# Kernel optimization log

Hardware: AMD Instinct MI355X
Metric: run time of the kernel (lower is better)

The kernel has to match this reference:

```python
import jax, jax.numpy as jnp
import numpy as np
import math

D_MODEL = 1024
NUM_HEADS = 16
HEAD_DIM = D_MODEL // NUM_HEADS


def setup_inputs() -> dict:
    key = jax.random.key(0)
    ks = jax.random.split(key, 9)
    B, S = 2, 2048
    scale = 1.0 / math.sqrt(D_MODEL)
    x = jax.random.normal(ks[0], (B, S, D_MODEL), dtype=jnp.float32)
    # torch nn.Linear params: weight [out, in], bias [out]
    Wq = jax.random.normal(ks[1], (D_MODEL, D_MODEL), dtype=jnp.float32) * scale
    bq = jax.random.normal(ks[2], (D_MODEL,), dtype=jnp.float32) * scale
    Wk = jax.random.normal(ks[3], (D_MODEL, D_MODEL), dtype=jnp.float32) * scale
    bk = jax.random.normal(ks[4], (D_MODEL,), dtype=jnp.float32) * scale
    Wv = jax.random.normal(ks[5], (D_MODEL, D_MODEL), dtype=jnp.float32) * scale
    bv = jax.random.normal(ks[6], (D_MODEL,), dtype=jnp.float32) * scale
    Wo = jax.random.normal(ks[7], (D_MODEL, D_MODEL), dtype=jnp.float32) * scale
    bo = jax.random.normal(ks[8], (D_MODEL,), dtype=jnp.float32) * scale
    return {"x": x, "Wq": Wq, "bq": bq, "Wk": Wk, "bk": bk,
            "Wv": Wv, "bv": bv, "Wo": Wo, "bo": bo}


def reference(x, Wq, bq, Wk, bk, Wv, bv, Wo, bo):
    B, S, _ = x.shape
    H, Dh = NUM_HEADS, HEAD_DIM

    def proj(W, b):
        # torch Linear: x @ W.T + b -> [B,S,D] -> [B,H,S,Dh]
        y = jnp.einsum('bsd,ed->bse', x, W) + b
        return y.reshape(B, S, H, Dh).transpose(0, 2, 1, 3)

    Q = proj(Wq, bq)
    K = proj(Wk, bk)
    V = proj(Wv, bv)

    # scores [B,H,S,S], causal mask with -inf, then scale by 1/sqrt(head_dim)
    scores = jnp.einsum('bhqd,bhkd->bhqk', Q, K)
    causal = jnp.tril(jnp.ones((S, S), dtype=bool))
    scores = jnp.where(causal, scores, -jnp.inf)
    A = jax.nn.softmax(scores / math.sqrt(Dh), axis=-1)

    O = jnp.einsum('bhqk,bhkd->bhqd', A, V)  # [B,H,S,Dh]
    O = O.transpose(0, 2, 1, 3).reshape(B, S, H * Dh)
    return jnp.einsum('bsd,ed->bse', O, Wo) + bo
```

## Files before the change

### kernel.cpp

```cpp
#include <hip/hip_runtime.h>


typedef _Float16 f16x8 __attribute__((ext_vector_type(8)));
typedef _Float16 f16x4 __attribute__((ext_vector_type(4)));
typedef _Float16 f16x2 __attribute__((ext_vector_type(2)));
typedef float f32x4 __attribute__((ext_vector_type(4)));

#define S_  2048
#define DM  1024
#define NH  16
#define DH  64

__device__ __forceinline__ void gload_lds16(const void* g, void* s) {
  __builtin_amdgcn_global_load_lds(
      (const __attribute__((address_space(1))) void*)g,
      (__attribute__((address_space(3))) void*)s, 16, 0, 0);
}

__device__ __forceinline__ f16x2 pkrtz(float a, float b) {
  return __builtin_bit_cast(f16x2, __builtin_amdgcn_cvt_pkrtz(a, b));
}


__global__ void cvt_x_kernel(const float* __restrict__ src,
                             _Float16* __restrict__ dst) {
  const int i = blockIdx.x * 256 + threadIdx.x;
  const float4 v = ((const float4*)src)[i];
  f16x4 h;
  h[0] = (_Float16)v.x; h[1] = (_Float16)v.y;
  h[2] = (_Float16)v.z; h[3] = (_Float16)v.w;
  ((f16x4*)dst)[i] = h;
}

__global__ void cvt_w_kernel(const float* __restrict__ w0,
                             const float* __restrict__ w1,
                             const float* __restrict__ w2,
                             const float* __restrict__ w3,
                             _Float16* __restrict__ dst) {
  const int y = blockIdx.y;
  const float* src = (y == 0) ? w0 : (y == 1) ? w1 : (y == 2) ? w2 : w3;
  const int i = blockIdx.x * 256 + threadIdx.x;
  const float4 v = ((const float4*)src)[i];
  f16x4 h;
  h[0] = (_Float16)v.x; h[1] = (_Float16)v.y;
  h[2] = (_Float16)v.z; h[3] = (_Float16)v.w;
  ((f16x4*)(dst + (size_t)y * (DM * DM)))[i] = h;
}


__device__ __forceinline__ void gemm_core_k1024(
    const _Float16* __restrict__ A, const _Float16* __restrict__ W,
    _Float16* As, _Float16* Ws, f32x4 acc[4][4], int m0, int n0)
{
  const int t = threadIdx.x;
  const int w = t >> 6, l = t & 63;
  const int quad = l >> 4, ln = l & 15;
  const int wm = (w >> 1) << 6, wn = (w & 1) << 6;
  const int srow = l >> 2, scol = (l & 3) << 3;

  for (int k0 = 0; k0 < DM; k0 += 32) {
#pragma unroll
    for (int i = 0; i < 2; ++i) {
      const int ra = w * 32 + i * 16;
      gload_lds16(&A[(size_t)(m0 + ra + srow) * DM + k0 + scol], &As[ra * 32]);
      gload_lds16(&W[(size_t)(n0 + ra + srow) * DM + k0 + scol], &Ws[ra * 32]);
    }
    __syncthreads();

    f16x8 af[4], bf[4];
#pragma unroll
    for (int mi = 0; mi < 4; ++mi)
      af[mi] = *(const f16x8*)&As[(wm + mi * 16 + ln) * 32 + quad * 8];
#pragma unroll
    for (int ni = 0; ni < 4; ++ni)
      bf[ni] = *(const f16x8*)&Ws[(wn + ni * 16 + ln) * 32 + quad * 8];
#pragma unroll
    for (int mi = 0; mi < 4; ++mi)
#pragma unroll
      for (int ni = 0; ni < 4; ++ni)
        acc[mi][ni] = __builtin_amdgcn_mfma_f32_16x16x32_f16(
            af[mi], bf[ni], acc[mi][ni], 0, 0, 0);
    __syncthreads();
  }
}

__global__ __launch_bounds__(256, 2) void gemm_qkv_kernel(
    const _Float16* __restrict__ xb, const _Float16* __restrict__ wb,
    const float* __restrict__ bq, const float* __restrict__ bk,
    const float* __restrict__ bv, _Float16* __restrict__ qkv)
{
  __shared__ _Float16 As[128 * 32];
  __shared__ _Float16 Ws[128 * 32];
  const int z = blockIdx.z;
  const _Float16* W = wb + (size_t)z * (DM * DM);
  const float* bias = (z == 0) ? bq : ((z == 1) ? bk : bv);
  _Float16* out = qkv + (size_t)z * 4194304;

  const f32x4 z4 = {0.f, 0.f, 0.f, 0.f};
  f32x4 acc[4][4];
#pragma unroll
  for (int mi = 0; mi < 4; ++mi)
#pragma unroll
    for (int ni = 0; ni < 4; ++ni) acc[mi][ni] = z4;

  const int m0 = blockIdx.y * 128, n0 = blockIdx.x * 128;
  gemm_core_k1024(xb, W, As, Ws, acc, m0, n0);

  const int t = threadIdx.x, w = t >> 6, l = t & 63;
  const int quad = l >> 4, ln = l & 15;
  const int wm = (w >> 1) << 6, wn = (w & 1) << 6;
  const float scale = (z == 0) ? 0.18033688f : 1.0f;

#pragma unroll
  for (int ni = 0; ni < 4; ++ni) {
    const int c = n0 + wn + ni * 16 + ln;
    const float bias_c = bias[c];
    const int h = c >> 6, d = c & 63;
#pragma unroll
    for (int mi = 0; mi < 4; ++mi) {
      const int mb = m0 + wm + mi * 16 + quad * 4;
#pragma unroll
      for (int r = 0; r < 4; ++r) {
        const int mg = mb + r;
        const int b = mg >> 11, s = mg & 2047;
        const int bh = b * NH + h;
        const float v = (acc[mi][ni][r] + bias_c) * scale;
        size_t idx;
        if (z == 2)
          idx = (size_t)bh * 131072 + (s >> 5) * 2048 + (d >> 4) * 512 +
                ((s >> 3) & 3) * 128 + (d & 15) * 8 + (s & 7);
        else
          idx = (size_t)bh * 131072 + (s >> 4) * 1024 + (d >> 5) * 512 +
                ((d >> 3) & 3) * 128 + (s & 15) * 8 + (d & 7);
        out[idx] = (_Float16)v;
      }
    }
  }
}

__global__ __launch_bounds__(256, 2) void gemm_out_kernel(
    const _Float16* __restrict__ ob, const _Float16* __restrict__ wo,
    const float* __restrict__ bo, float* __restrict__ out)
{
  __shared__ _Float16 As[128 * 32];
  __shared__ _Float16 Ws[128 * 32];
  const f32x4 z4 = {0.f, 0.f, 0.f, 0.f};
  f32x4 acc[4][4];
#pragma unroll
  for (int mi = 0; mi < 4; ++mi)
#pragma unroll
    for (int ni = 0; ni < 4; ++ni) acc[mi][ni] = z4;

  const int m0 = blockIdx.y * 128, n0 = blockIdx.x * 128;
  gemm_core_k1024(ob, wo, As, Ws, acc, m0, n0);

  const int t = threadIdx.x, w = t >> 6, l = t & 63;
  const int quad = l >> 4, ln = l & 15;
  const int wm = (w >> 1) << 6, wn = (w & 1) << 6;

#pragma unroll
  for (int ni = 0; ni < 4; ++ni) {
    const int c = n0 + wn + ni * 16 + ln;
    const float bias_c = bo[c];
#pragma unroll
    for (int mi = 0; mi < 4; ++mi) {
      const int mb = m0 + wm + mi * 16 + quad * 4;
#pragma unroll
      for (int r = 0; r < 4; ++r)
        out[(size_t)(mb + r) * DM + c] = acc[mi][ni][r] + bias_c;
    }
  }
}


struct KVfrag { f16x8 k[4]; f16x8 v[4]; };

__device__ __forceinline__ KVfrag load_tile(const _Float16* __restrict__ kb_,
                                            const _Float16* __restrict__ vb_,
                                            int t, int l) {
  KVfrag f;
#pragma unroll
  for (int i = 0; i < 4; ++i)
    f.k[i] = *(const f16x8*)(kb_ + (size_t)(t * 4 + i) * 512 + l * 8);
#pragma unroll
  for (int i = 0; i < 4; ++i)
    f.v[i] = *(const f16x8*)(vb_ + (size_t)(t * 4 + i) * 512 + l * 8);
  return f;
}

template <bool DIAG>
__device__ __forceinline__ void compute_tile(
    const KVfrag& kv, const f16x8 (&qf)[2][2], f32x4 (&oacc)[4][2],
    float (&l_i)[2], _Float16* Ps, int quad, int ln)
{
  const f32x4 z4 = {0.f, 0.f, 0.f, 0.f};
  f32x4 sacc[2][2];
#pragma unroll
  for (int mi = 0; mi < 2; ++mi)
#pragma unroll
    for (int qc = 0; qc < 2; ++qc) sacc[mi][qc] = z4;

#pragma unroll
  for (int ks = 0; ks < 2; ++ks)
#pragma unroll
    for (int mi = 0; mi < 2; ++mi)
#pragma unroll
      for (int qc = 0; qc < 2; ++qc)
        sacc[mi][qc] = __builtin_amdgcn_mfma_f32_16x16x32_f16(
            kv.k[mi * 2 + ks], qf[qc][ks], sacc[mi][qc], 0, 0, 0);

  const int sw = (ln & 3) << 1;
#pragma unroll
  for (int qc = 0; qc < 2; ++qc) {
    float rs = 0.f;
#pragma unroll
    for (int mi = 0; mi < 2; ++mi) {
      float p[4];
#pragma unroll
      for (int r = 0; r < 4; ++r) {
        p[r] = __builtin_amdgcn_exp2f(sacc[mi][qc][r]);
        if (DIAG && (mi * 16 + quad * 4 + r > qc * 16 + ln)) p[r] = 0.f;
        rs += p[r];
      }
      const f16x2 lo = pkrtz(p[0], p[1]);
      const f16x2 hi = pkrtz(p[2], p[3]);
      const f16x4 pk = __builtin_shufflevector(lo, hi, 0, 1, 2, 3);
      const int g = (mi * 4 + quad) ^ sw;
      *(f16x4*)&Ps[(qc * 16 + ln) * 40 + g * 4] = pk;
    }
    rs += __shfl_xor(rs, 16);
    rs += __shfl_xor(rs, 32);
    l_i[qc] += rs;
  }

  f16x8 pb[2];
#pragma unroll
  for (int qc = 0; qc < 2; ++qc) {
    const int g2 = (quad * 2) ^ sw;
    pb[qc] = *(const f16x8*)&Ps[(qc * 16 + ln) * 40 + g2 * 4];
  }

#pragma unroll
  for (int di = 0; di < 4; ++di)
#pragma unroll
    for (int qc = 0; qc < 2; ++qc)
      oacc[di][qc] = __builtin_amdgcn_mfma_f32_16x16x32_f16(
          kv.v[di], pb[qc], oacc[di][qc], 0, 0, 0);
}

__global__ __launch_bounds__(128, 2) void attn_kernel(
    const _Float16* __restrict__ QF, const _Float16* __restrict__ KF,
    const _Float16* __restrict__ VF, _Float16* __restrict__ Ob)
{
  __shared__ _Float16 Ps[2 * 32 * 40];
  __shared__ float mrg[64 * 34];

  const int i = blockIdx.x;
  const int bh = ((i & 7) << 2) | ((i >> 3) & 3);
  const int p = i >> 5;

  const int tid = threadIdx.x;
  const int w = tid >> 6, l = tid & 63;
  const int quad = l >> 4, ln = l & 15;

  const _Float16* qb_ = QF + (size_t)bh * 131072;
  const _Float16* kb_ = KF + (size_t)bh * 131072;
  const _Float16* vb_ = VF + (size_t)bh * 131072;
  _Float16* psw = Ps + w * (32 * 40);
  const int bidx = bh >> 4, h = bh & 15;

  const f32x4 z4 = {0.f, 0.f, 0.f, 0.f};

#pragma unroll
  for (int mem = 0; mem < 2; ++mem) {
    const int qw = (mem == 0) ? (63 - p) : p;
    const int q0 = qw << 5;

    f16x8 qf[2][2];
#pragma unroll
    for (int qc = 0; qc < 2; ++qc)
#pragma unroll
      for (int ks = 0; ks < 2; ++ks)
        qf[qc][ks] = *(const f16x8*)
            (qb_ + (size_t)((2 * qw + qc) * 2 + ks) * 512 + l * 8);

    f32x4 oacc[4][2];
#pragma unroll
    for (int di = 0; di < 4; ++di)
#pragma unroll
      for (int qc = 0; qc < 2; ++qc) oacc[di][qc] = z4;
    float l_i[2] = {0.f, 0.f};

    const int n = (qw >= w) ? (((qw - w) >> 1) + 1) : 0;
    if (n > 0) {
      KVfrag b0 = load_tile(kb_, vb_, w, l);
      KVfrag b1;
      for (int k = 0; k + 1 < n; ++k) {
        const int tnext = w + 2 * (k + 1);
        if ((k & 1) == 0) {
          b1 = load_tile(kb_, vb_, tnext, l);
          compute_tile<false>(b0, qf, oacc, l_i, psw, quad, ln);
        } else {
          b0 = load_tile(kb_, vb_, tnext, l);
          compute_tile<false>(b1, qf, oacc, l_i, psw, quad, ln);
        }
      }
      const KVfrag& last = ((n - 1) & 1) ? b1 : b0;
      if (((qw - w) & 1) == 0)
        compute_tile<true>(last, qf, oacc, l_i, psw, quad, ln);
      else
        compute_tile<false>(last, qf, oacc, l_i, psw, quad, ln);
    }

    if (w == 1) {
#pragma unroll
      for (int di = 0; di < 4; ++di)
#pragma unroll
        for (int qc = 0; qc < 2; ++qc)
#pragma unroll
          for (int r = 0; r < 4; ++r)
            mrg[l * 34 + di * 8 + qc * 4 + r] = oacc[di][qc][r];
#pragma unroll
      for (int qc = 0; qc < 2; ++qc) mrg[l * 34 + 32 + qc] = l_i[qc];
    }
    __syncthreads();
    if (w == 0) {
#pragma unroll
      for (int qc = 0; qc < 2; ++qc) {
        const float inv = 1.0f / (l_i[qc] + mrg[l * 34 + 32 + qc]);
        const int q = q0 + qc * 16 + ln;
        _Float16* orow = Ob + (size_t)(bidx * S_ + q) * DM + h * DH + quad * 4;
#pragma unroll
        for (int di = 0; di < 4; ++di) {
          f16x4 o4;
#pragma unroll
          for (int r = 0; r < 4; ++r)
            o4[r] = (_Float16)((oacc[di][qc][r] +
                                mrg[l * 34 + di * 8 + qc * 4 + r]) * inv);
          *(f16x4*)(orow + di * 16) = o4;
        }
      }
    }
    __syncthreads();
  }
}


extern "C" void kernel_launch(void* const* d_in, const int* in_sizes, int n_in,
                              void* d_out, int out_size, void* d_ws, size_t ws_size,
                              hipStream_t stream) {
  (void)in_sizes; (void)n_in; (void)out_size; (void)ws_size;
  const float* x  = (const float*)d_in[0];
  const float* Wq = (const float*)d_in[1];
  const float* bq = (const float*)d_in[2];
  const float* Wk = (const float*)d_in[3];
  const float* bk = (const float*)d_in[4];
  const float* Wv = (const float*)d_in[5];
  const float* bv = (const float*)d_in[6];
  const float* Wo = (const float*)d_in[7];
  const float* bo = (const float*)d_in[8];

  char* ws = (char*)d_ws;
  _Float16* xb  = (_Float16*)(ws);
  _Float16* wb  = (_Float16*)(ws + (8u << 20));
  _Float16* qkv = (_Float16*)(ws + (16u << 20));
  _Float16* ob  = (_Float16*)(ws + (40u << 20));

  cvt_x_kernel<<<dim3(4096), dim3(256), 0, stream>>>(x, xb);
  cvt_w_kernel<<<dim3(1024, 4), dim3(256), 0, stream>>>(Wq, Wk, Wv, Wo, wb);
  gemm_qkv_kernel<<<dim3(8, 32, 3), dim3(256), 0, stream>>>(xb, wb, bq, bk, bv, qkv);
  attn_kernel<<<dim3(1024), dim3(128), 0, stream>>>(
      qkv, qkv + 4194304, qkv + 2 * 4194304, ob);
  gemm_out_kernel<<<dim3(8, 32), dim3(256), 0, stream>>>(
      ob, wb + (size_t)3 * DM * DM, bo, (float*)d_out);
}
```

Before: 185.0 us.

## Split attention KV across four waves and split-K the output GEMM with atomics

```diff
diff --git a/kernel.cpp b/kernel.cpp
--- a/kernel.cpp
+++ b/kernel.cpp
@@ -47,10 +47,17 @@
   ((f16x4*)(dst + (size_t)y * (DM * DM)))[i] = h;
 }
 
-
-__device__ __forceinline__ void gemm_core_k1024(
+__global__ void bias_fill_kernel(const float* __restrict__ bo,
+                                 float* __restrict__ out) {
+  const int i = blockIdx.x * 256 + threadIdx.x;
+  ((float4*)out)[i] = ((const float4*)bo)[i & 255];
+}
+
+
+__device__ __forceinline__ void gemm_core(
     const _Float16* __restrict__ A, const _Float16* __restrict__ W,
-    _Float16* As, _Float16* Ws, f32x4 acc[4][4], int m0, int n0)
+    _Float16* As, _Float16* Ws, f32x4 acc[4][4], int m0, int n0,
+    int kbeg, int kend)
 {
   const int t = threadIdx.x;
   const int w = t >> 6, l = t & 63;
@@ -58,7 +65,7 @@
   const int wm = (w >> 1) << 6, wn = (w & 1) << 6;
   const int srow = l >> 2, scol = (l & 3) << 3;
 
-  for (int k0 = 0; k0 < DM; k0 += 32) {
+  for (int k0 = kbeg; k0 < kend; k0 += 32) {
 #pragma unroll
     for (int i = 0; i < 2; ++i) {
       const int ra = w * 32 + i * 16;
@@ -104,7 +111,7 @@
     for (int ni = 0; ni < 4; ++ni) acc[mi][ni] = z4;
 
   const int m0 = blockIdx.y * 128, n0 = blockIdx.x * 128;
-  gemm_core_k1024(xb, W, As, Ws, acc, m0, n0);
+  gemm_core(xb, W, As, Ws, acc, m0, n0, 0, DM);
 
   const int t = threadIdx.x, w = t >> 6, l = t & 63;
   const int quad = l >> 4, ln = l & 15;
@@ -140,7 +147,7 @@
 
 __global__ __launch_bounds__(256, 2) void gemm_out_kernel(
     const _Float16* __restrict__ ob, const _Float16* __restrict__ wo,
-    const float* __restrict__ bo, float* __restrict__ out)
+    float* __restrict__ out)
 {
   __shared__ _Float16 As[128 * 32];
   __shared__ _Float16 Ws[128 * 32];
@@ -152,7 +159,8 @@
     for (int ni = 0; ni < 4; ++ni) acc[mi][ni] = z4;
 
   const int m0 = blockIdx.y * 128, n0 = blockIdx.x * 128;
-  gemm_core_k1024(ob, wo, As, Ws, acc, m0, n0);
+  const int kbeg = blockIdx.z * 512;
+  gemm_core(ob, wo, As, Ws, acc, m0, n0, kbeg, kbeg + 512);
 
   const int t = threadIdx.x, w = t >> 6, l = t & 63;
   const int quad = l >> 4, ln = l & 15;
@@ -161,13 +169,12 @@
 #pragma unroll
   for (int ni = 0; ni < 4; ++ni) {
     const int c = n0 + wn + ni * 16 + ln;
-    const float bias_c = bo[c];
 #pragma unroll
     for (int mi = 0; mi < 4; ++mi) {
       const int mb = m0 + wm + mi * 16 + quad * 4;
 #pragma unroll
       for (int r = 0; r < 4; ++r)
-        out[(size_t)(mb + r) * DM + c] = acc[mi][ni][r] + bias_c;
+        atomicAdd(&out[(size_t)(mb + r) * DM + c], acc[mi][ni][r]);
     }
   }
 }
@@ -228,8 +235,6 @@
       const int g = (mi * 4 + quad) ^ sw;
       *(f16x4*)&Ps[(qc * 16 + ln) * 40 + g * 4] = pk;
     }
-    rs += __shfl_xor(rs, 16);
-    rs += __shfl_xor(rs, 32);
     l_i[qc] += rs;
   }
 
@@ -248,12 +253,12 @@
           kv.v[di], pb[qc], oacc[di][qc], 0, 0, 0);
 }
 
-__global__ __launch_bounds__(128, 2) void attn_kernel(
+__global__ __launch_bounds__(256, 4) void attn_kernel(
     const _Float16* __restrict__ QF, const _Float16* __restrict__ KF,
     const _Float16* __restrict__ VF, _Float16* __restrict__ Ob)
 {
-  __shared__ _Float16 Ps[2 * 32 * 40];
-  __shared__ float mrg[64 * 34];
+  __shared__ _Float16 Ps[4 * 32 * 40];
+  __shared__ float mrg[3 * 64 * 36];
 
   const int i = blockIdx.x;
   const int bh = ((i & 7) << 2) | ((i >> 3) & 3);
@@ -291,12 +296,12 @@
       for (int qc = 0; qc < 2; ++qc) oacc[di][qc] = z4;
     float l_i[2] = {0.f, 0.f};
 
-    const int n = (qw >= w) ? (((qw - w) >> 1) + 1) : 0;
+    const int n = (qw >= w) ? (((qw - w) >> 2) + 1) : 0;
     if (n > 0) {
       KVfrag b0 = load_tile(kb_, vb_, w, l);
       KVfrag b1;
       for (int k = 0; k + 1 < n; ++k) {
-        const int tnext = w + 2 * (k + 1);
+        const int tnext = w + 4 * (k + 1);
         if ((k & 1) == 0) {
           b1 = load_tile(kb_, vb_, tnext, l);
           compute_tile<false>(b0, qf, oacc, l_i, psw, quad, ln);
@@ -306,28 +311,46 @@
         }
       }
       const KVfrag& last = ((n - 1) & 1) ? b1 : b0;
-      if (((qw - w) & 1) == 0)
+      if (((qw - w) & 3) == 0)
         compute_tile<true>(last, qf, oacc, l_i, psw, quad, ln);
       else
         compute_tile<false>(last, qf, oacc, l_i, psw, quad, ln);
     }
 
-    if (w == 1) {
+#pragma unroll
+    for (int qc = 0; qc < 2; ++qc) {
+      float s = l_i[qc];
+      s += __shfl_xor(s, 16);
+      s += __shfl_xor(s, 32);
+      l_i[qc] = s;
+    }
+
+    if (w != 0) {
+      float* m_ = &mrg[((w - 1) * 64 + l) * 36];
 #pragma unroll
       for (int di = 0; di < 4; ++di)
 #pragma unroll
         for (int qc = 0; qc < 2; ++qc)
-#pragma unroll
-          for (int r = 0; r < 4; ++r)
-            mrg[l * 34 + di * 8 + qc * 4 + r] = oacc[di][qc][r];
-#pragma unroll
-      for (int qc = 0; qc < 2; ++qc) mrg[l * 34 + 32 + qc] = l_i[qc];
+          *(f32x4*)(m_ + di * 8 + qc * 4) = oacc[di][qc];
+      m_[32] = l_i[0];
+      m_[33] = l_i[1];
     }
     __syncthreads();
     if (w == 0) {
 #pragma unroll
+      for (int ww = 0; ww < 3; ++ww) {
+        const float* m_ = &mrg[(ww * 64 + l) * 36];
+#pragma unroll
+        for (int di = 0; di < 4; ++di)
+#pragma unroll
+          for (int qc = 0; qc < 2; ++qc)
+            oacc[di][qc] += *(const f32x4*)(m_ + di * 8 + qc * 4);
+        l_i[0] += m_[32];
+        l_i[1] += m_[33];
+      }
+#pragma unroll
       for (int qc = 0; qc < 2; ++qc) {
-        const float inv = 1.0f / (l_i[qc] + mrg[l * 34 + 32 + qc]);
+        const float inv = 1.0f / l_i[qc];
         const int q = q0 + qc * 16 + ln;
         _Float16* orow = Ob + (size_t)(bidx * S_ + q) * DM + h * DH + quad * 4;
 #pragma unroll
@@ -335,8 +358,7 @@
           f16x4 o4;
 #pragma unroll
           for (int r = 0; r < 4; ++r)
-            o4[r] = (_Float16)((oacc[di][qc][r] +
-                                mrg[l * 34 + di * 8 + qc * 4 + r]) * inv);
+            o4[r] = (_Float16)(oacc[di][qc][r] * inv);
           *(f16x4*)(orow + di * 16) = o4;
         }
       }
@@ -368,9 +390,10 @@
 
   cvt_x_kernel<<<dim3(4096), dim3(256), 0, stream>>>(x, xb);
   cvt_w_kernel<<<dim3(1024, 4), dim3(256), 0, stream>>>(Wq, Wk, Wv, Wo, wb);
+  bias_fill_kernel<<<dim3(4096), dim3(256), 0, stream>>>(bo, (float*)d_out);
   gemm_qkv_kernel<<<dim3(8, 32, 3), dim3(256), 0, stream>>>(xb, wb, bq, bk, bv, qkv);
-  attn_kernel<<<dim3(1024), dim3(128), 0, stream>>>(
+  attn_kernel<<<dim3(1024), dim3(256), 0, stream>>>(
       qkv, qkv + 4194304, qkv + 2 * 4194304, ob);
-  gemm_out_kernel<<<dim3(8, 32), dim3(256), 0, stream>>>(
-      ob, wb + (size_t)3 * DM * DM, bo, (float*)d_out);
-}
+  gemm_out_kernel<<<dim3(8, 32, 2), dim3(256), 0, stream>>>(
+      ob, wb + (size_t)3 * DM * DM, (float*)d_out);
+}
```

Measured after the change: 458.8 us. 148% more time.
